# Performance work log

Hardware: AMD Instinct MI355X
Metric: run time of the kernel (lower is better)

## Reference

```python
import math
import jax, jax.numpy as jnp
import numpy as np

N_HEADS = 16
HIDDEN = 1024
FACTOR = 256
N_DK = HIDDEN // N_HEADS
B, S = 4, 2048


def _linear_params(key, fan_in, fan_out):
    kw, kb = jax.random.split(key)
    bound = 1.0 / math.sqrt(fan_in)
    W = jax.random.uniform(kw, (fan_in, fan_out), jnp.float32, -bound, bound)
    b = jax.random.uniform(kb, (fan_out,), jnp.float32, -bound, bound)
    return W, b


def setup_inputs() -> dict:
    key = jax.random.key(0)
    ks = jax.random.split(key, 12)
    inp = {
        "query": jax.random.normal(ks[0], (B, S, HIDDEN), jnp.float32),
        "key": jax.random.normal(ks[1], (B, S, HIDDEN), jnp.float32),
        "value": jax.random.normal(ks[2], (B, S, HIDDEN), jnp.float32),
        "mask": jax.random.randint(ks[3], (B, S), 0, 2, jnp.int32),
    }
    names = [("pq", HIDDEN, FACTOR), ("tq", FACTOR, HIDDEN),
             ("pk", HIDDEN, FACTOR), ("tk", FACTOR, HIDDEN),
             ("pv", HIDDEN, FACTOR), ("tv", FACTOR, HIDDEN),
             ("po", HIDDEN, FACTOR), ("to", FACTOR, HIDDEN)]
    for i, (nm, fi, fo) in enumerate(names):
        W, b = _linear_params(ks[4 + i], fi, fo)
        inp[f"W{nm}"], inp[f"b{nm}"] = W, b
    return inp


def _factored(x, Wp, bp, Wt, bt):
    # proj -> leaky_relu(0.2) -> tran
    h = jax.nn.leaky_relu(x @ Wp + bp, negative_slope=0.2)
    return h @ Wt + bt


def reference(query, key, value, mask,
              Wpq, bpq, Wtq, btq, Wpk, bpk, Wtk, btk,
              Wpv, bpv, Wtv, btv, Wpo, bpo, Wto, bto):
    bsize = query.shape[0]

    def split_heads(x):  # [B,S,H*Dk] -> [B,H,S,Dk]
        return x.reshape(bsize, -1, N_HEADS, N_DK).transpose(0, 2, 1, 3)

    q = split_heads(_factored(query, Wpq, bpq, Wtq, btq))
    k = split_heads(_factored(key, Wpk, bpk, Wtk, btk))
    v = split_heads(_factored(value, Wpv, bpv, Wtv, btv))

    scores = jnp.einsum("bhqd,bhkd->bhqk", q, k) / math.sqrt(N_DK)
    m = (mask == 0)[:, None, None, :]  # [B,1,1,S]
    scores = jnp.where(m, jnp.float32(-1e20), scores)
    attn = jax.nn.softmax(scores, axis=-1)
    cv = jnp.einsum("bhqk,bhkd->bhqd", attn, v)
    cv = cv.transpose(0, 2, 1, 3).reshape(bsize, -1, N_HEADS * N_DK)
    # dropout omitted (eval mode / deterministic reference)
    return _factored(cv, Wpo, bpo, Wto, bto)
```

## Files before the change

kernel.cpp:

```cpp
#include <hip/hip_runtime.h>
#include <cstdint>
#include <cstddef>

typedef __bf16 bf16_t;
typedef __bf16 bf16x8 __attribute__((ext_vector_type(8)));
typedef float  f32x4  __attribute__((ext_vector_type(4)));
typedef unsigned int uint32x4 __attribute__((ext_vector_type(4)));
typedef unsigned int uint32x2 __attribute__((ext_vector_type(2)));

#define DEV_INLINE __device__ __forceinline__

constexpr int Bsz = 4, Ssz = 2048, HID = 1024, FAC = 256, NH = 16, DKc = 64;
constexpr int Mrows = Bsz * Ssz;
constexpr float QSCALE = 0.18033688011112042f;

struct Ptr8 { const float* p[8]; };
struct Ptr3 { const float* p[3]; };

DEV_INLINE float fast_exp2(float x) {
#if __has_builtin(__builtin_amdgcn_exp2f)
  return __builtin_amdgcn_exp2f(x);
#else
  return exp2f(x);
#endif
}

DEV_INLINE void async16(const void* g, void* l) {
  __builtin_amdgcn_global_load_lds((const __attribute__((address_space(1))) void*)g,
                                   (__attribute__((address_space(3))) void*)l, 16, 0, 0);
}

DEV_INLINE int SW(int r) { return (r & 3) | ((r >> 1) & 4); }

__global__ __launch_bounds__(256) void k_prep(Ptr8 w, Ptr8 bsrc, const int* __restrict__ mask,
                                              bf16_t* wpt, bf16_t* wtt,
                                              float* bp, float* bt, float* mf, bf16_t* mb) {
  const int z = blockIdx.z;
  if (z == 8) {
    const int bid = blockIdx.y * 32 + blockIdx.x;
    if (bid >= 64) return;
    const int i = bid * 256 + threadIdx.x;
    if (i < 4 * FAC) bp[i] = bsrc.p[i >> 8][i & 255];
    if (i < 4 * HID) bt[i] = bsrc.p[4 + (i >> 10)][i & 1023];
    if (i < Bsz * Ssz) {
      const float m = (mask[i] != 0) ? 1.f : 0.f;
      mf[i] = m;
      mb[i] = (bf16_t)m;
    }
    return;
  }
  const int K = (z < 4) ? HID : FAC;
  const int N = (z < 4) ? FAC : HID;
  if ((int)(blockIdx.x * 32) >= N || (int)(blockIdx.y * 32) >= K) return;
  __shared__ float t[32][33];
  const float* src = w.p[z];
  bf16_t* dst = (z < 4) ? (wpt + (size_t)z * FAC * HID) : (wtt + (size_t)(z - 4) * FAC * HID);
  const int tx = threadIdx.x & 31, ty = threadIdx.x >> 5;
  const int kb = blockIdx.y * 32, nb = blockIdx.x * 32;
#pragma unroll
  for (int j = 0; j < 4; ++j)
    t[ty + j * 8][tx] = src[(size_t)(kb + ty + j * 8) * N + nb + tx];
  __syncthreads();
#pragma unroll
  for (int j = 0; j < 4; ++j)
    dst[(size_t)(nb + ty + j * 8) * K + kb + tx] = (bf16_t)t[tx][ty + j * 8];
}

template <int CAST_A, typename OUT_T>
__global__ __launch_bounds__(256) void k_gemmP(Ptr3 Asrc,
                                               const bf16_t* __restrict__ Aall,
                                               const bf16_t* __restrict__ Bt_,
                                               const float* __restrict__ biasAll,
                                               OUT_T* __restrict__ Call,
                                               int K,
                                               long long Az, long long Bz, long long Cz, int biasz) {
  constexpr int LDTA = CAST_A ? 40 : 32;
  __shared__ __align__(16) bf16_t As[2][64 * LDTA];
  __shared__ __align__(16) bf16_t Bs[2][128 * 32];

  const int z = blockIdx.z;
  const bf16_t* Bt = Bt_ + (size_t)z * Bz;
  const float* bias = biasAll + (size_t)z * biasz;
  OUT_T* C = Call + (size_t)z * Cz;

  const int tid = threadIdx.x;
  const int lane = tid & 63, wave = tid >> 6;
  const int quad = lane >> 4, l16 = lane & 15;
  const int m0 = blockIdx.y * 64, n0 = blockIdx.x * 128;

  const int arow = wave * 16 + (lane >> 2), akc = (lane & 3) * 8;
  const bf16_t* gB0 = Bt + (size_t)(n0 + arow) * K + akc;
  const bf16_t* gB1 = gB0 + (size_t)64 * K;

  const float* gAf = nullptr;
  const bf16_t* gA = nullptr;
  const int crow = tid >> 2, chalf = (tid & 3) * 8;
  if (CAST_A) gAf = Asrc.p[z] + (size_t)(m0 + crow) * K + chalf;
  else        gA  = Aall + (size_t)z * Az + (size_t)(m0 + arow) * K + akc;

  async16(gB0, Bs[0] + wave * 512);
  async16(gB1, Bs[0] + 2048 + wave * 512);
  if (CAST_A) {
    f32x4 x0 = *(const f32x4*)gAf;
    f32x4 x1 = *(const f32x4*)(gAf + 4);
    union { bf16_t h[8]; uint32x4 u; } o;
#pragma unroll
    for (int j = 0; j < 4; ++j) { o.h[j] = (bf16_t)x0[j]; o.h[4 + j] = (bf16_t)x1[j]; }
    *(uint32x4*)(As[0] + crow * LDTA + chalf) = o.u;
  } else {
    async16(gA, As[0] + wave * 512);
  }

  f32x4 acc[4][2] = {};
  const int nk = K / 32;

  for (int it = 0; it < nk; ++it) {
    const int cur = it & 1, nxt = cur ^ 1;
    __syncthreads();

    f32x4 xa, xb;
    const int k1 = (it + 1) * 32;
    if (it + 1 < nk) {
      async16(gB0 + k1, Bs[nxt] + wave * 512);
      async16(gB1 + k1, Bs[nxt] + 2048 + wave * 512);
      if (CAST_A) {
        xa = *(const f32x4*)(gAf + k1);
        xb = *(const f32x4*)(gAf + k1 + 4);
      } else {
        async16(gA + k1, As[nxt] + wave * 512);
      }
    }

    bf16x8 af[4], bfr[2];
#pragma unroll
    for (int i = 0; i < 4; ++i)
      af[i] = *(const bf16x8*)(As[cur] + (i * 16 + l16) * LDTA + quad * 8);
#pragma unroll
    for (int i = 0; i < 2; ++i)
      bfr[i] = *(const bf16x8*)(Bs[cur] + (wave * 32 + i * 16 + l16) * 32 + quad * 8);
#pragma unroll
    for (int mi = 0; mi < 4; ++mi)
#pragma unroll
      for (int ni = 0; ni < 2; ++ni)
        acc[mi][ni] = __builtin_amdgcn_mfma_f32_16x16x32_bf16(af[mi], bfr[ni], acc[mi][ni], 0, 0, 0);

    if (CAST_A && it + 1 < nk) {
      union { bf16_t h[8]; uint32x4 u; } o;
#pragma unroll
      for (int j = 0; j < 4; ++j) { o.h[j] = (bf16_t)xa[j]; o.h[4 + j] = (bf16_t)xb[j]; }
      *(uint32x4*)(As[nxt] + crow * LDTA + chalf) = o.u;
    }
  }

#pragma unroll
  for (int mi = 0; mi < 4; ++mi) {
    const int rbase = m0 + mi * 16 + quad * 4;
#pragma unroll
    for (int ni = 0; ni < 2; ++ni) {
      const int col = n0 + wave * 32 + ni * 16 + l16;
      const float bv = bias[col];
#pragma unroll
      for (int r = 0; r < 4; ++r) {
        float y = acc[mi][ni][r] + bv;
        y = (y > 0.f) ? y : 0.2f * y;
        C[(size_t)(rbase + r) * FAC + col] = (OUT_T)y;
      }
    }
  }
}

template <int TVW, typename OUT_T>
__global__ __launch_bounds__(256) void k_gemm(const bf16_t* __restrict__ Aall,
                                              const bf16_t* __restrict__ Btall,
                                              const float* __restrict__ biasAll,
                                              OUT_T* __restrict__ Call,
                                              bf16_t* __restrict__ C2,
                                              const float* __restrict__ rowmul,
                                              int N, int K,
                                              long long Az, long long Bz, long long Cz, int biasz,
                                              float sc0, float sc1) {
  __shared__ __align__(16) bf16_t As[128 * 32];
  __shared__ __align__(16) bf16_t Bs[128 * 32];

  const int z = blockIdx.z;
  const bf16_t* Bt = Btall + (size_t)z * Bz;
  const float* bias = biasAll + (size_t)z * biasz;
  OUT_T* C = Call + (size_t)z * Cz;
  const float scale = (z == 0) ? sc0 : sc1;

  const int tid = threadIdx.x;
  const int lane = tid & 63, wave = tid >> 6;
  const int quad = lane >> 4, l16 = lane & 15;
  const int wr = wave >> 1, wc = wave & 1;
  const int m0 = blockIdx.y * 128, n0 = blockIdx.x * 128;

  const int arow = wave * 16 + (lane >> 2), akc = (lane & 3) * 8;
  const bf16_t* gB0 = Bt + (size_t)(n0 + arow) * K + akc;
  const bf16_t* gB1 = gB0 + (size_t)64 * K;
  bf16_t* lB0 = Bs + wave * 512;
  bf16_t* lB1 = Bs + 2048 + wave * 512;

  const bf16_t* A = Aall + (size_t)z * Az;
  const bf16_t* gA0 = A + (size_t)(m0 + arow) * K + akc;
  const bf16_t* gA1 = gA0 + (size_t)64 * K;
  bf16_t* lA0 = As + wave * 512;
  bf16_t* lA1 = As + 2048 + wave * 512;

  f32x4 acc[4][4] = {};

  for (int k0 = 0; k0 < K; k0 += 32) {
    async16(gB0 + k0, lB0);
    async16(gB1 + k0, lB1);
    async16(gA0 + k0, lA0);
    async16(gA1 + k0, lA1);
    __syncthreads();

    bf16x8 af[4], bfr[4];
#pragma unroll
    for (int i = 0; i < 4; ++i)
      af[i] = *(const bf16x8*)(As + (wr * 64 + i * 16 + l16) * 32 + quad * 8);
#pragma unroll
    for (int i = 0; i < 4; ++i)
      bfr[i] = *(const bf16x8*)(Bs + (wc * 64 + i * 16 + l16) * 32 + quad * 8);
#pragma unroll
    for (int mi = 0; mi < 4; ++mi)
#pragma unroll
      for (int ni = 0; ni < 4; ++ni)
        acc[mi][ni] = __builtin_amdgcn_mfma_f32_16x16x32_bf16(af[mi], bfr[ni], acc[mi][ni], 0, 0, 0);
    if (k0 + 32 < K) __syncthreads();
  }

  if (TVW && z == 2) {
#pragma unroll
    for (int mi = 0; mi < 4; ++mi) {
      const int rbase = m0 + wr * 64 + mi * 16 + quad * 4;
      const int bb = rbase >> 11, s = rbase & 2047;
      float rmv[4];
#pragma unroll
      for (int r = 0; r < 4; ++r) rmv[r] = rowmul[rbase + r];
#pragma unroll
      for (int ni = 0; ni < 4; ++ni) {
        const int col = n0 + wc * 64 + ni * 16 + l16;
        const float bv = bias[col];
        const int h = col >> 6, d = col & 63;
        union { bf16_t e[4]; uint32x2 u; } p;
#pragma unroll
        for (int r = 0; r < 4; ++r) p.e[r] = (bf16_t)((acc[mi][ni][r] + bv) * rmv[r]);
        *(uint32x2*)(C2 + (((size_t)((bb * NH + h) * DKc + d)) << 11) + s) = p.u;
      }
    }
    return;
  }

#pragma unroll
  for (int mi = 0; mi < 4; ++mi) {
    const int rbase = m0 + wr * 64 + mi * 16 + quad * 4;
#pragma unroll
    for (int ni = 0; ni < 4; ++ni) {
      const int col = n0 + wc * 64 + ni * 16 + l16;
      const float bv = bias[col];
#pragma unroll
      for (int r = 0; r < 4; ++r) {
        float y = (acc[mi][ni][r] + bv) * scale;
        C[(size_t)(rbase + r) * N + col] = (OUT_T)y;
      }
    }
  }
}

__global__ __launch_bounds__(256, 2) void k_attn(const bf16_t* __restrict__ qkv,
                                                 const bf16_t* __restrict__ mb,
                                                 bf16_t* __restrict__ cv) {
  __shared__ __align__(16) bf16_t Ks[2][64 * 64];
  __shared__ __align__(16) bf16_t Vt[2][64 * 64];
  __shared__ __align__(16) bf16_t Ml[Ssz];

  const int qt = blockIdx.x, h = blockIdx.y, b = blockIdx.z;
  const bf16_t* qp = qkv;
  const bf16_t* kp = qkv + (size_t)Mrows * HID;
  const bf16_t* vtp = qkv + 2 * (size_t)Mrows * HID + (size_t)(b * NH + h) * DKc * Ssz;

  const int tid = threadIdx.x;
  const int lane = tid & 63, wave = tid >> 6;
  const int quad = lane >> 4, l16 = lane & 15;

  const int r0 = wave * 16 + (lane >> 3);
  const int r1 = r0 + 8;
  const int c0 = ((lane & 7) ^ SW(r0)) * 8;
  const int c1 = ((lane & 7) ^ SW(r1)) * 8;
  const int ldsOff = wave * 1024;
  const bf16_t* kgA = kp + (size_t)(b * Ssz + r0) * HID + h * DKc + c0;
  const bf16_t* kgB = kp + (size_t)(b * Ssz + r1) * HID + h * DKc + c1;
  const bf16_t* vgA = vtp + (size_t)r0 * Ssz + c0;
  const bf16_t* vgB = vtp + (size_t)r1 * Ssz + c1;

  *(uint32x4*)(Ml + tid * 8) = *(const uint32x4*)(mb + (size_t)b * Ssz + tid * 8);
  async16(kgA, Ks[0] + ldsOff);
  async16(kgB, Ks[0] + ldsOff + 512);
  async16(vgA, Vt[0] + ldsOff);
  async16(vgB, Vt[0] + ldsOff + 512);

  bf16x8 aq0[4], aq1[4];
#pragma unroll
  for (int g = 0; g < 4; ++g) {
    const size_t qrow = (size_t)(b * Ssz + qt * 256 + g * 64 + wave * 16 + l16) * HID + h * DKc + quad * 8;
    aq0[g] = *(const bf16x8*)(qp + qrow);
    aq1[g] = *(const bf16x8*)(qp + qrow + 32);
  }
  __syncthreads();

  const int krow = 8 * (l16 >> 2) + (l16 & 3);
  f32x4 acc[4][4] = {};
  f32x4 dacc[4] = {};
  const bf16x8 zfrag = {};

  for (int kt = 0; kt < 32; ++kt) {
    const int cur = kt & 1, nxt = cur ^ 1;
    if (kt < 31) {
      const size_t ko = (size_t)(kt + 1) * 64 * HID;
      const int vo = (kt + 1) * 64;
      async16(kgA + ko, Ks[nxt] + ldsOff);
      async16(kgB + ko, Ks[nxt] + ldsOff + 512);
      async16(vgA + vo, Vt[nxt] + ldsOff);
      async16(vgB + vo, Vt[nxt] + ldsOff + 512);
    }

    union U { uint32x4 u; bf16x8 h; } ap0[4], ap1[4];
    constexpr int koff[4] = {0, 4, 32, 36};
#pragma unroll
    for (int ks = 0; ks < 4; ++ks) {
      const int row = krow + koff[ks];
      const int sw = SW(row);
      bf16x8 a0 = *(const bf16x8*)(Ks[cur] + row * 64 + (quad ^ sw) * 8);
      bf16x8 a1 = *(const bf16x8*)(Ks[cur] + row * 64 + ((quad + 4) ^ sw) * 8);
#pragma unroll
      for (int g = 0; g < 4; ++g) {
        f32x4 c = {};
        c = __builtin_amdgcn_mfma_f32_16x16x32_bf16(a0, aq0[g], c, 0, 0, 0);
        c = __builtin_amdgcn_mfma_f32_16x16x32_bf16(a1, aq1[g], c, 0, 0, 0);
        union { bf16_t h[2]; uint32_t u; } p01, p23;
        p01.h[0] = (bf16_t)fast_exp2(c[0]);
        p01.h[1] = (bf16_t)fast_exp2(c[1]);
        p23.h[0] = (bf16_t)fast_exp2(c[2]);
        p23.h[1] = (bf16_t)fast_exp2(c[3]);
        U& t = (ks < 2) ? ap0[g] : ap1[g];
        t.u[(ks & 1) * 2] = p01.u;
        t.u[(ks & 1) * 2 + 1] = p23.u;
      }
    }

    bf16x8 mr0 = *(const bf16x8*)(Ml + kt * 64 + quad * 8);
    bf16x8 mr1 = *(const bf16x8*)(Ml + kt * 64 + 32 + quad * 8);
    if (l16 != 0) { mr0 = zfrag; mr1 = zfrag; }
#pragma unroll
    for (int g = 0; g < 4; ++g) {
      dacc[g] = __builtin_amdgcn_mfma_f32_16x16x32_bf16(ap0[g].h, mr0, dacc[g], 0, 0, 0);
      dacc[g] = __builtin_amdgcn_mfma_f32_16x16x32_bf16(ap1[g].h, mr1, dacc[g], 0, 0, 0);
    }

#pragma unroll
    for (int d = 0; d < 4; ++d) {
      const int row = d * 16 + l16;
      const int sw = SW(row);
      bf16x8 bv0 = *(const bf16x8*)(Vt[cur] + row * 64 + (quad ^ sw) * 8);
      bf16x8 bv1 = *(const bf16x8*)(Vt[cur] + row * 64 + ((quad + 4) ^ sw) * 8);
#pragma unroll
      for (int g = 0; g < 4; ++g) {
        acc[g][d] = __builtin_amdgcn_mfma_f32_16x16x32_bf16(ap0[g].h, bv0, acc[g][d], 0, 0, 0);
        acc[g][d] = __builtin_amdgcn_mfma_f32_16x16x32_bf16(ap1[g].h, bv1, acc[g][d], 0, 0, 0);
      }
    }

    __syncthreads();
  }

#pragma unroll
  for (int g = 0; g < 4; ++g) {
    const size_t obase = (size_t)(b * Ssz + qt * 256 + g * 64 + wave * 16 + quad * 4) * HID + h * DKc + l16;
#pragma unroll
    for (int r = 0; r < 4; ++r) {
      const float denom = __shfl(dacc[g][r], lane & 48, 64);
      const float rl = 1.f / denom;
#pragma unroll
      for (int d = 0; d < 4; ++d)
        cv[obase + (size_t)r * HID + d * 16] = (bf16_t)(acc[g][d][r] * rl);
    }
  }
}

extern "C" void kernel_launch(void* const* d_in, const int* in_sizes, int n_in,
                              void* d_out, int out_size, void* d_ws, size_t ws_size,
                              hipStream_t stream) {
  (void)in_sizes; (void)n_in; (void)out_size; (void)ws_size;
  const float* q_in = (const float*)d_in[0];
  const float* k_in = (const float*)d_in[1];
  const float* v_in = (const float*)d_in[2];
  const int* mask = (const int*)d_in[3];

  bf16_t* XB = (bf16_t*)d_ws;
  bf16_t* H3 = XB + (size_t)3 * Mrows * HID;
  bf16_t* CV = H3 + (size_t)3 * Mrows * FAC;
  bf16_t* WPT = CV + (size_t)Mrows * HID;
  bf16_t* WTT = WPT + (size_t)4 * FAC * HID;
  float* BP = (float*)(WTT + (size_t)4 * FAC * HID);
  float* BT = BP + 4 * FAC;
  float* MF = BT + 4 * HID;
  bf16_t* MB = (bf16_t*)(MF + Mrows);
  bf16_t* VTg = XB + 2 * (size_t)Mrows * HID;

  Ptr8 w;
  w.p[0] = (const float*)d_in[4];  w.p[1] = (const float*)d_in[8];
  w.p[2] = (const float*)d_in[12]; w.p[3] = (const float*)d_in[16];
  w.p[4] = (const float*)d_in[6];  w.p[5] = (const float*)d_in[10];
  w.p[6] = (const float*)d_in[14]; w.p[7] = (const float*)d_in[18];
  Ptr8 bs;
  bs.p[0] = (const float*)d_in[5];  bs.p[1] = (const float*)d_in[9];
  bs.p[2] = (const float*)d_in[13]; bs.p[3] = (const float*)d_in[17];
  bs.p[4] = (const float*)d_in[7];  bs.p[5] = (const float*)d_in[11];
  bs.p[6] = (const float*)d_in[15]; bs.p[7] = (const float*)d_in[19];
  hipLaunchKernelGGL(k_prep, dim3(32, 32, 9), dim3(256), 0, stream, w, bs, mask,
                     WPT, WTT, BP, BT, MF, MB);

  Ptr3 xs; xs.p[0] = q_in; xs.p[1] = k_in; xs.p[2] = v_in;
  Ptr3 nullp; nullp.p[0] = nullp.p[1] = nullp.p[2] = nullptr;

  hipLaunchKernelGGL((k_gemmP<1, bf16_t>), dim3(2, Mrows / 64, 3), dim3(256), 0, stream,
                     xs, (const bf16_t*)nullptr, WPT, BP, H3,
                     HID, 0LL, (long long)FAC * HID, (long long)Mrows * FAC, FAC);

  hipLaunchKernelGGL((k_gemm<1, bf16_t>), dim3(HID / 128, Mrows / 128, 3), dim3(256), 0, stream,
                     H3, WTT, BT, XB, VTg, MF,
                     HID, FAC, (long long)Mrows * FAC, (long long)FAC * HID, (long long)Mrows * HID, HID,
                     QSCALE, 1.f);

  hipLaunchKernelGGL(k_attn, dim3(Ssz / 256, NH, Bsz), dim3(256), 0, stream, XB, MB, CV);

  hipLaunchKernelGGL((k_gemmP<0, bf16_t>), dim3(2, Mrows / 64, 1), dim3(256), 0, stream,
                     nullp, CV, WPT + (size_t)3 * FAC * HID, BP + 3 * FAC, H3,
                     HID, 0LL, 0LL, 0LL, 0);

  hipLaunchKernelGGL((k_gemm<0, float>), dim3(HID / 128, Mrows / 128, 1), dim3(256), 0, stream,
                     H3, WTT + (size_t)3 * FAC * HID, BT + 3 * HID, (float*)d_out, (bf16_t*)nullptr,
                     (const float*)nullptr, HID, FAC, 0LL, 0LL, 0LL, 0, 1.f, 1.f);
}
```

Baseline: 349.9 us.

## Double-buffer GEMM LDS tiles and split attention work across eight waves

The k_gemm main loop now double-buffers the A/B shared tiles. The next k-slice is issued asynchronously after the barrier, so each iteration needs one barrier instead of two and loads overlap the MFMAs. The attention kernel moves from 4 waves to 8 waves per block, with each wave handling two query groups instead of four. This halves per-wave accumulator registers and spreads the K/V tile loads across more threads, aiming for more latency hiding and occupancy. In exchange, the shared K/V tile is reused by fewer query rows per wave, so LDS reads per MFMA rise.

```diff
diff --git a/kernel.cpp b/kernel.cpp
--- a/kernel.cpp
+++ b/kernel.cpp
@@ -179,8 +179,8 @@
                                               int N, int K,
                                               long long Az, long long Bz, long long Cz, int biasz,
                                               float sc0, float sc1) {
-  __shared__ __align__(16) bf16_t As[128 * 32];
-  __shared__ __align__(16) bf16_t Bs[128 * 32];
+  __shared__ __align__(16) bf16_t As[2][128 * 32];
+  __shared__ __align__(16) bf16_t Bs[2][128 * 32];
 
   const int z = blockIdx.z;
   const bf16_t* Bt = Btall + (size_t)z * Bz;
@@ -197,37 +197,42 @@
   const int arow = wave * 16 + (lane >> 2), akc = (lane & 3) * 8;
   const bf16_t* gB0 = Bt + (size_t)(n0 + arow) * K + akc;
   const bf16_t* gB1 = gB0 + (size_t)64 * K;
-  bf16_t* lB0 = Bs + wave * 512;
-  bf16_t* lB1 = Bs + 2048 + wave * 512;
-
   const bf16_t* A = Aall + (size_t)z * Az;
   const bf16_t* gA0 = A + (size_t)(m0 + arow) * K + akc;
   const bf16_t* gA1 = gA0 + (size_t)64 * K;
-  bf16_t* lA0 = As + wave * 512;
-  bf16_t* lA1 = As + 2048 + wave * 512;
+
+  async16(gB0, Bs[0] + wave * 512);
+  async16(gB1, Bs[0] + 2048 + wave * 512);
+  async16(gA0, As[0] + wave * 512);
+  async16(gA1, As[0] + 2048 + wave * 512);
 
   f32x4 acc[4][4] = {};
-
-  for (int k0 = 0; k0 < K; k0 += 32) {
-    async16(gB0 + k0, lB0);
-    async16(gB1 + k0, lB1);
-    async16(gA0 + k0, lA0);
-    async16(gA1 + k0, lA1);
+  const int nk = K / 32;
+
+  for (int it = 0; it < nk; ++it) {
+    const int cur = it & 1, nxt = cur ^ 1;
     __syncthreads();
 
+    if (it + 1 < nk) {
+      const int k1 = (it + 1) * 32;
+      async16(gB0 + k1, Bs[nxt] + wave * 512);
+      async16(gB1 + k1, Bs[nxt] + 2048 + wave * 512);
+      async16(gA0 + k1, As[nxt] + wave * 512);
+      async16(gA1 + k1, As[nxt] + 2048 + wave * 512);
+    }
+
     bf16x8 af[4], bfr[4];
 #pragma unroll
     for (int i = 0; i < 4; ++i)
-      af[i] = *(const bf16x8*)(As + (wr * 64 + i * 16 + l16) * 32 + quad * 8);
+      af[i] = *(const bf16x8*)(As[cur] + (wr * 64 + i * 16 + l16) * 32 + quad * 8);
 #pragma unroll
     for (int i = 0; i < 4; ++i)
-      bfr[i] = *(const bf16x8*)(Bs + (wc * 64 + i * 16 + l16) * 32 + quad * 8);
+      bfr[i] = *(const bf16x8*)(Bs[cur] + (wc * 64 + i * 16 + l16) * 32 + quad * 8);
 #pragma unroll
     for (int mi = 0; mi < 4; ++mi)
 #pragma unroll
       for (int ni = 0; ni < 4; ++ni)
         acc[mi][ni] = __builtin_amdgcn_mfma_f32_16x16x32_bf16(af[mi], bfr[ni], acc[mi][ni], 0, 0, 0);
-    if (k0 + 32 < K) __syncthreads();
   }
 
   if (TVW && z == 2) {
@@ -268,7 +273,7 @@
   }
 }
 
-__global__ __launch_bounds__(256, 2) void k_attn(const bf16_t* __restrict__ qkv,
+__global__ __launch_bounds__(512, 4) void k_attn(const bf16_t* __restrict__ qkv,
                                                  const bf16_t* __restrict__ mb,
                                                  bf16_t* __restrict__ cv) {
   __shared__ __align__(16) bf16_t Ks[2][64 * 64];
@@ -284,34 +289,28 @@
   const int lane = tid & 63, wave = tid >> 6;
   const int quad = lane >> 4, l16 = lane & 15;
 
-  const int r0 = wave * 16 + (lane >> 3);
-  const int r1 = r0 + 8;
+  const int r0 = wave * 8 + (lane >> 3);
   const int c0 = ((lane & 7) ^ SW(r0)) * 8;
-  const int c1 = ((lane & 7) ^ SW(r1)) * 8;
-  const int ldsOff = wave * 1024;
+  const int ldsOff = wave * 512;
   const bf16_t* kgA = kp + (size_t)(b * Ssz + r0) * HID + h * DKc + c0;
-  const bf16_t* kgB = kp + (size_t)(b * Ssz + r1) * HID + h * DKc + c1;
   const bf16_t* vgA = vtp + (size_t)r0 * Ssz + c0;
-  const bf16_t* vgB = vtp + (size_t)r1 * Ssz + c1;
-
-  *(uint32x4*)(Ml + tid * 8) = *(const uint32x4*)(mb + (size_t)b * Ssz + tid * 8);
+
+  *(uint32x2*)(Ml + tid * 4) = *(const uint32x2*)(mb + (size_t)b * Ssz + tid * 4);
   async16(kgA, Ks[0] + ldsOff);
-  async16(kgB, Ks[0] + ldsOff + 512);
   async16(vgA, Vt[0] + ldsOff);
-  async16(vgB, Vt[0] + ldsOff + 512);
-
-  bf16x8 aq0[4], aq1[4];
-#pragma unroll
-  for (int g = 0; g < 4; ++g) {
-    const size_t qrow = (size_t)(b * Ssz + qt * 256 + g * 64 + wave * 16 + l16) * HID + h * DKc + quad * 8;
+
+  bf16x8 aq0[2], aq1[2];
+#pragma unroll
+  for (int g = 0; g < 2; ++g) {
+    const size_t qrow = (size_t)(b * Ssz + qt * 256 + g * 128 + wave * 16 + l16) * HID + h * DKc + quad * 8;
     aq0[g] = *(const bf16x8*)(qp + qrow);
     aq1[g] = *(const bf16x8*)(qp + qrow + 32);
   }
   __syncthreads();
 
   const int krow = 8 * (l16 >> 2) + (l16 & 3);
-  f32x4 acc[4][4] = {};
-  f32x4 dacc[4] = {};
+  f32x4 acc[2][4] = {};
+  f32x4 dacc[2] = {};
   const bf16x8 zfrag = {};
 
   for (int kt = 0; kt < 32; ++kt) {
@@ -320,12 +319,10 @@
       const size_t ko = (size_t)(kt + 1) * 64 * HID;
       const int vo = (kt + 1) * 64;
       async16(kgA + ko, Ks[nxt] + ldsOff);
-      async16(kgB + ko, Ks[nxt] + ldsOff + 512);
       async16(vgA + vo, Vt[nxt] + ldsOff);
-      async16(vgB + vo, Vt[nxt] + ldsOff + 512);
-    }
-
-    union U { uint32x4 u; bf16x8 h; } ap0[4], ap1[4];
+    }
+
+    union U { uint32x4 u; bf16x8 h; } ap0[2], ap1[2];
     constexpr int koff[4] = {0, 4, 32, 36};
 #pragma unroll
     for (int ks = 0; ks < 4; ++ks) {
@@ -334,7 +331,7 @@
       bf16x8 a0 = *(const bf16x8*)(Ks[cur] + row * 64 + (quad ^ sw) * 8);
       bf16x8 a1 = *(const bf16x8*)(Ks[cur] + row * 64 + ((quad + 4) ^ sw) * 8);
 #pragma unroll
-      for (int g = 0; g < 4; ++g) {
+      for (int g = 0; g < 2; ++g) {
         f32x4 c = {};
         c = __builtin_amdgcn_mfma_f32_16x16x32_bf16(a0, aq0[g], c, 0, 0, 0);
         c = __builtin_amdgcn_mfma_f32_16x16x32_bf16(a1, aq1[g], c, 0, 0, 0);
@@ -353,7 +350,7 @@
     bf16x8 mr1 = *(const bf16x8*)(Ml + kt * 64 + 32 + quad * 8);
     if (l16 != 0) { mr0 = zfrag; mr1 = zfrag; }
 #pragma unroll
-    for (int g = 0; g < 4; ++g) {
+    for (int g = 0; g < 2; ++g) {
       dacc[g] = __builtin_amdgcn_mfma_f32_16x16x32_bf16(ap0[g].h, mr0, dacc[g], 0, 0, 0);
       dacc[g] = __builtin_amdgcn_mfma_f32_16x16x32_bf16(ap1[g].h, mr1, dacc[g], 0, 0, 0);
     }
@@ -365,7 +362,7 @@
       bf16x8 bv0 = *(const bf16x8*)(Vt[cur] + row * 64 + (quad ^ sw) * 8);
       bf16x8 bv1 = *(const bf16x8*)(Vt[cur] + row * 64 + ((quad + 4) ^ sw) * 8);
 #pragma unroll
-      for (int g = 0; g < 4; ++g) {
+      for (int g = 0; g < 2; ++g) {
         acc[g][d] = __builtin_amdgcn_mfma_f32_16x16x32_bf16(ap0[g].h, bv0, acc[g][d], 0, 0, 0);
         acc[g][d] = __builtin_amdgcn_mfma_f32_16x16x32_bf16(ap1[g].h, bv1, acc[g][d], 0, 0, 0);
       }
@@ -375,8 +372,8 @@
   }
 
 #pragma unroll
-  for (int g = 0; g < 4; ++g) {
-    const size_t obase = (size_t)(b * Ssz + qt * 256 + g * 64 + wave * 16 + quad * 4) * HID + h * DKc + l16;
+  for (int g = 0; g < 2; ++g) {
+    const size_t obase = (size_t)(b * Ssz + qt * 256 + g * 128 + wave * 16 + quad * 4) * HID + h * DKc + l16;
 #pragma unroll
     for (int r = 0; r < 4; ++r) {
       const float denom = __shfl(dacc[g][r], lane & 48, 64);
@@ -433,7 +430,7 @@
                      HID, FAC, (long long)Mrows * FAC, (long long)FAC * HID, (long long)Mrows * HID, HID,
                      QSCALE, 1.f);
 
-  hipLaunchKernelGGL(k_attn, dim3(Ssz / 256, NH, Bsz), dim3(256), 0, stream, XB, MB, CV);
+  hipLaunchKernelGGL(k_attn, dim3(Ssz / 256, NH, Bsz), dim3(512), 0, stream, XB, MB, CV);
 
   hipLaunchKernelGGL((k_gemmP<0, bf16_t>), dim3(2, Mrows / 64, 1), dim3(256), 0, stream,
                      nullp, CV, WPT + (size_t)3 * FAC * HID, BP + 3 * FAC, H3,
```

Result: faster. 340.6 us (-2.7%).
